# Kernel tuning notes

Hardware: AMD Instinct MI355X
Metric: run time of the kernel (lower is better)

Reference implementation:

```python
import jax, jax.numpy as jnp
import numpy as np

B, N, F, E = 4, 4096, 64, 64
EPS = 1e-5  # torch LayerNorm default

def setup_inputs() -> dict:
    key = jax.random.key(0)
    k = jax.random.split(key, 5)
    x = jax.random.normal(k[0], (B, N, F), dtype=jnp.float32)
    # LayerNorm affine params
    ln_gamma = jnp.ones((F,), dtype=jnp.float32)
    ln_beta = jnp.zeros((F,), dtype=jnp.float32)
    # Stacked Linear(1, E) weights/biases: proj_w[i] == param_projectors[i].weight[:, 0]
    bound = 1.0  # kaiming_uniform for fan_in=1 -> U(-1, 1); bias U(-1, 1) as well
    proj_w = jax.random.uniform(k[1], (F, E), dtype=jnp.float32, minval=-bound, maxval=bound)
    proj_b = jax.random.uniform(k[2], (F, E), dtype=jnp.float32, minval=-bound, maxval=bound)
    param_embeddings = 0.02 * jax.random.normal(k[3], (F, E), dtype=jnp.float32)
    return {"x": x, "ln_gamma": ln_gamma, "ln_beta": ln_beta,
            "proj_w": proj_w, "proj_b": proj_b, "param_embeddings": param_embeddings}

def reference(x, ln_gamma, ln_beta, proj_w, proj_b, param_embeddings):
    # LayerNorm over last dim (feature_dim)
    mu = jnp.mean(x, axis=-1, keepdims=True)
    var = jnp.mean(jnp.square(x - mu), axis=-1, keepdims=True)
    xn = (x - mu) * jax.lax.rsqrt(var + EPS) * ln_gamma + ln_beta  # [B,N,F]
    # Per-feature scalar -> E projection fused: out[b,n,f,e] = xn[b,n,f]*w[f,e] + b[f,e] + emb[f,e]
    out = xn[..., None] * proj_w + (proj_b + param_embeddings)  # [B,N,F,E]
    Bs, Ns, Fs, Es = out.shape
    return out.reshape(Bs, Ns, Fs * Es)
```

## Files before the change

### kernel.cpp

```cpp
#include <hip/hip_runtime.h>

#define LN_EPS 1e-5f


__global__ __launch_bounds__(256) void pte_kernel(
    const float* __restrict__ x,
    const float* __restrict__ gamma,
    const float* __restrict__ beta,
    const float* __restrict__ w,
    const float* __restrict__ pb,
    const float* __restrict__ emb,
    float* __restrict__ out)
{
    const int row = blockIdx.x;
    const int tid = threadIdx.x;

    __shared__ float xn_s[64];

    if (tid < 64) {
        float v = x[(size_t)row * 64 + tid];

        float s = v;
        #pragma unroll
        for (int m = 1; m < 64; m <<= 1) s += __shfl_xor(s, m, 64);
        float mu = s * (1.0f / 64.0f);

        float d = v - mu;
        float s2 = d * d;
        #pragma unroll
        for (int m = 1; m < 64; m <<= 1) s2 += __shfl_xor(s2, m, 64);
        float inv = rsqrtf(s2 * (1.0f / 64.0f) + LN_EPS);

        xn_s[tid] = d * inv * gamma[tid] + beta[tid];
    }
    __syncthreads();

    const float4* __restrict__ w4 = (const float4*)w;
    const float4* __restrict__ b4 = (const float4*)pb;
    const float4* __restrict__ e4 = (const float4*)emb;
    float4* __restrict__ o4 = (float4*)(out + (size_t)row * 4096);

    #pragma unroll
    for (int i = 0; i < 4; ++i) {
        int idx = i * 256 + tid;
        int f = idx >> 4;
        float xn = xn_s[f];
        float4 wv = w4[idx];
        float4 bv = b4[idx];
        float4 ev = e4[idx];
        float4 r;
        r.x = fmaf(xn, wv.x, bv.x + ev.x);
        r.y = fmaf(xn, wv.y, bv.y + ev.y);
        r.z = fmaf(xn, wv.z, bv.z + ev.z);
        r.w = fmaf(xn, wv.w, bv.w + ev.w);
        o4[idx] = r;
    }
}

extern "C" void kernel_launch(void* const* d_in, const int* in_sizes, int n_in,
                              void* d_out, int out_size, void* d_ws, size_t ws_size,
                              hipStream_t stream) {
    const float* x     = (const float*)d_in[0];
    const float* gamma = (const float*)d_in[1];
    const float* beta  = (const float*)d_in[2];
    const float* w     = (const float*)d_in[3];
    const float* pb    = (const float*)d_in[4];
    const float* emb   = (const float*)d_in[5];
    float* out = (float*)d_out;

    const int rows = 4 * 4096;
    pte_kernel<<<rows, 256, 0, stream>>>(x, gamma, beta, w, pb, emb, out);
}
```

Measured before the change: 54.16 us.

## Use persistent blocks with register-cached weights and redundant per-wave LayerNorm

Switches to a grid-stride persistent kernel with 2048 blocks. Each thread loads its w and the combined bias+embedding float4 slices into registers once and reuses them across rows. Every wave now computes the LayerNorm redundantly and broadcasts normalized values via __shfl, which removes the shared-memory buffer and __syncthreads. The next row's x is prefetched while the current row is being processed. This cuts repeated parameter loads and barrier cost, in exchange for more registers and redundant reduction work per wave.

```diff
diff --git a/kernel.cpp b/kernel.cpp
--- a/kernel.cpp
+++ b/kernel.cpp
@@ -10,50 +10,63 @@
     const float* __restrict__ w,
     const float* __restrict__ pb,
     const float* __restrict__ emb,
-    float* __restrict__ out)
+    float* __restrict__ out,
+    int rows)
 {
-    const int row = blockIdx.x;
-    const int tid = threadIdx.x;
+    const int tid  = threadIdx.x;
+    const int lane = tid & 63;
+    const int wave = tid >> 6;
 
-    __shared__ float xn_s[64];
+    const float4* __restrict__ w4 = (const float4*)w;
+    const float4* __restrict__ b4 = (const float4*)pb;
+    const float4* __restrict__ e4 = (const float4*)emb;
 
-    if (tid < 64) {
-        float v = x[(size_t)row * 64 + tid];
+    float4 wv[4], cv[4];
+    #pragma unroll
+    for (int i = 0; i < 4; ++i) {
+        int idx = i * 256 + tid;
+        wv[i] = w4[idx];
+        float4 bv = b4[idx], ev = e4[idx];
+        cv[i].x = bv.x + ev.x;
+        cv[i].y = bv.y + ev.y;
+        cv[i].z = bv.z + ev.z;
+        cv[i].w = bv.w + ev.w;
+    }
+    const float g  = gamma[lane];
+    const float bt = beta[lane];
 
+    const int fbase = wave * 4 + (lane >> 4);
+
+    int row = blockIdx.x;
+    float v = (row < rows) ? x[(size_t)row * 64 + lane] : 0.0f;
+
+    for (; row < rows; row += gridDim.x) {
         float s = v;
         #pragma unroll
         for (int m = 1; m < 64; m <<= 1) s += __shfl_xor(s, m, 64);
         float mu = s * (1.0f / 64.0f);
-
-        float d = v - mu;
+        float d  = v - mu;
         float s2 = d * d;
         #pragma unroll
         for (int m = 1; m < 64; m <<= 1) s2 += __shfl_xor(s2, m, 64);
         float inv = rsqrtf(s2 * (1.0f / 64.0f) + LN_EPS);
+        float xn_lane = d * inv * g + bt;
 
-        xn_s[tid] = d * inv * gamma[tid] + beta[tid];
-    }
-    __syncthreads();
+        int nrow = row + gridDim.x;
+        float vn = (nrow < rows) ? x[(size_t)nrow * 64 + lane] : 0.0f;
 
-    const float4* __restrict__ w4 = (const float4*)w;
-    const float4* __restrict__ b4 = (const float4*)pb;
-    const float4* __restrict__ e4 = (const float4*)emb;
-    float4* __restrict__ o4 = (float4*)(out + (size_t)row * 4096);
-
-    #pragma unroll
-    for (int i = 0; i < 4; ++i) {
-        int idx = i * 256 + tid;
-        int f = idx >> 4;
-        float xn = xn_s[f];
-        float4 wv = w4[idx];
-        float4 bv = b4[idx];
-        float4 ev = e4[idx];
-        float4 r;
-        r.x = fmaf(xn, wv.x, bv.x + ev.x);
-        r.y = fmaf(xn, wv.y, bv.y + ev.y);
-        r.z = fmaf(xn, wv.z, bv.z + ev.z);
-        r.w = fmaf(xn, wv.w, bv.w + ev.w);
-        o4[idx] = r;
+        float4* __restrict__ o4 = (float4*)(out + (size_t)row * 4096);
+        #pragma unroll
+        for (int i = 0; i < 4; ++i) {
+            float xn = __shfl(xn_lane, i * 16 + fbase, 64);
+            float4 r;
+            r.x = fmaf(xn, wv[i].x, cv[i].x);
+            r.y = fmaf(xn, wv[i].y, cv[i].y);
+            r.z = fmaf(xn, wv[i].z, cv[i].z);
+            r.w = fmaf(xn, wv[i].w, cv[i].w);
+            o4[i * 256 + tid] = r;
+        }
+        v = vn;
     }
 }
 
@@ -69,5 +82,6 @@
     float* out = (float*)d_out;
 
     const int rows = 4 * 4096;
-    pte_kernel<<<rows, 256, 0, stream>>>(x, gamma, beta, w, pb, emb, out);
+    const int grid = 2048;
+    pte_kernel<<<grid, 256, 0, stream>>>(x, gamma, beta, w, pb, emb, out, rows);
 }
```

After: 57.63 us. 1.06x slower.

## Compute LayerNorm per wavefront with shuffles, drop shared memory and barrier, nontemporal stores

Applied to the files above, without the earlier changes.

Every wavefront now recomputes the row's LayerNorm statistics itself, using a single-pass sum and sum-of-squares reduction, and gets each feature's normalized value through a lane shuffle. This removes the shared-memory staging and the __syncthreads barrier. Weight, bias and embedding loads are issued before the reduction so their latency overlaps it. Output writes use nontemporal stores to limit cache pollution. The cost is four times the reduction work per block and a slightly less numerically stable variance formula.

```diff
diff --git a/kernel.cpp b/kernel.cpp
--- a/kernel.cpp
+++ b/kernel.cpp
@@ -2,6 +2,8 @@
 
 #define LN_EPS 1e-5f
 
+
+typedef float f4 __attribute__((ext_vector_type(4)));
 
 __global__ __launch_bounds__(256) void pte_kernel(
     const float* __restrict__ x,
@@ -12,48 +14,51 @@
     const float* __restrict__ emb,
     float* __restrict__ out)
 {
-    const int row = blockIdx.x;
-    const int tid = threadIdx.x;
+    const int row  = blockIdx.x;
+    const int tid  = threadIdx.x;
+    const int lane = tid & 63;
 
-    __shared__ float xn_s[64];
+    const f4* __restrict__ w4 = (const f4*)w;
+    const f4* __restrict__ b4 = (const f4*)pb;
+    const f4* __restrict__ e4 = (const f4*)emb;
 
-    if (tid < 64) {
-        float v = x[(size_t)row * 64 + tid];
-
-        float s = v;
-        #pragma unroll
-        for (int m = 1; m < 64; m <<= 1) s += __shfl_xor(s, m, 64);
-        float mu = s * (1.0f / 64.0f);
-
-        float d = v - mu;
-        float s2 = d * d;
-        #pragma unroll
-        for (int m = 1; m < 64; m <<= 1) s2 += __shfl_xor(s2, m, 64);
-        float inv = rsqrtf(s2 * (1.0f / 64.0f) + LN_EPS);
-
-        xn_s[tid] = d * inv * gamma[tid] + beta[tid];
-    }
-    __syncthreads();
-
-    const float4* __restrict__ w4 = (const float4*)w;
-    const float4* __restrict__ b4 = (const float4*)pb;
-    const float4* __restrict__ e4 = (const float4*)emb;
-    float4* __restrict__ o4 = (float4*)(out + (size_t)row * 4096);
-
+    f4 wv[4], bv[4], ev[4];
     #pragma unroll
     for (int i = 0; i < 4; ++i) {
         int idx = i * 256 + tid;
-        int f = idx >> 4;
-        float xn = xn_s[f];
-        float4 wv = w4[idx];
-        float4 bv = b4[idx];
-        float4 ev = e4[idx];
-        float4 r;
-        r.x = fmaf(xn, wv.x, bv.x + ev.x);
-        r.y = fmaf(xn, wv.y, bv.y + ev.y);
-        r.z = fmaf(xn, wv.z, bv.z + ev.z);
-        r.w = fmaf(xn, wv.w, bv.w + ev.w);
-        o4[idx] = r;
+        wv[i] = w4[idx];
+        bv[i] = b4[idx];
+        ev[i] = e4[idx];
+    }
+
+    float v  = x[(size_t)row * 64 + lane];
+    float g  = gamma[lane];
+    float bt = beta[lane];
+
+    float s  = v;
+    float s2 = v * v;
+    #pragma unroll
+    for (int m = 1; m < 64; m <<= 1) {
+        s  += __shfl_xor(s,  m, 64);
+        s2 += __shfl_xor(s2, m, 64);
+    }
+    float mu  = s * (1.0f / 64.0f);
+    float var = fmaf(-mu, mu, s2 * (1.0f / 64.0f));
+    float inv = rsqrtf(var + LN_EPS);
+    float xn_lane = (v - mu) * inv * g + bt;
+
+    const int fbase = ((tid >> 6) << 2) + (lane >> 4);
+
+    f4* __restrict__ o4 = (f4*)(out + (size_t)row * 4096);
+    #pragma unroll
+    for (int i = 0; i < 4; ++i) {
+        float xn = __shfl(xn_lane, i * 16 + fbase, 64);
+        f4 r;
+        r.x = fmaf(xn, wv[i].x, bv[i].x + ev[i].x);
+        r.y = fmaf(xn, wv[i].y, bv[i].y + ev[i].y);
+        r.z = fmaf(xn, wv[i].z, bv[i].z + ev[i].z);
+        r.w = fmaf(xn, wv[i].w, bv[i].w + ev[i].w);
+        __builtin_nontemporal_store(r, &o4[i * 256 + tid]);
     }
 }
 
```

After: 51.05 us. -5.7%, faster.
